# Kernel tuning notes

Hardware: AMD Instinct MI355X
Metric: run time of the kernel (lower is better)

## Reference

```python
import jax, jax.numpy as jnp
import numpy as np

N_NODES = 50000   # num graph nodes
N_EDGES = 800000  # avg degree 16
D = 96            # in_channels == out_channels (residual aggr_out + x)


def setup_inputs() -> dict:
    key = jax.random.key(0)
    k0, k1, k2, k3, k4 = jax.random.split(key, 5)
    x = jax.random.normal(k0, (N_NODES, D), dtype=jnp.float32)
    edge_index = jax.random.randint(k1, (2, N_EDGES), 0, N_NODES)  # [2,E]: row0=src(j), row1=dst(i)
    edge_weight = jax.random.uniform(k2, (N_EDGES,), dtype=jnp.float32)
    pagerank = jax.random.uniform(k3, (N_NODES,), dtype=jnp.float32)
    # nn.Linear(in_channels, out_channels) params
    W = jax.random.normal(k4, (D, D), dtype=jnp.float32) / np.sqrt(D).astype(np.float32)
    b = jnp.zeros((D,), dtype=jnp.float32)
    return {"x": x, "edge_index": edge_index, "edge_weight": edge_weight,
            "pagerank": pagerank, "W": W, "b": b}


def reference(x, edge_index, edge_weight, pagerank, W, b):
    # CGCConv (PyG MessagePassing, aggr='add', flow source_to_target):
    #   message: edge_weight * x_j * pagerank_j   (gather from source nodes)
    #   aggregate: scatter-add to destination nodes
    #   update: Linear(aggr_out + x)
    src = edge_index[0]
    dst = edge_index[1]
    # [E, D] messages: per-edge gather-multiply
    msgs = edge_weight[:, None] * x[src] * pagerank[src][:, None]
    aggr = jax.ops.segment_sum(msgs, dst, num_segments=x.shape[0])  # [N, D]
    return (aggr + x) @ W.T + b
```

## Files before the change

### kernel.cpp

```cpp
#include <hip/hip_runtime.h>


constexpr int NN = 50000;
constexpr int NE = 800000;
constexpr int DD = 96;
constexpr int NB = 196;
constexpr int CAPB = 4608;
constexpr int EPB = 4096;
constexpr int NBLK = (NE + EPB - 1) / EPB;
constexpr int NCVT = (NN * DD / 4 + 511) / 512;

__device__ inline unsigned short f2bf(float f) {
    unsigned u = __float_as_uint(f);
    return (unsigned short)((u + 0x7FFFu + ((u >> 16) & 1u)) >> 16);
}
__device__ inline float bfh(unsigned short v) {
    return __uint_as_float((unsigned)v << 16);
}
__device__ inline unsigned long long pack_e(int meta, float c) {
    return (unsigned long long)(unsigned)meta |
           ((unsigned long long)(unsigned)__float_as_uint(c) << 32);
}

__global__ __launch_bounds__(256) void k_zero(int* __restrict__ cur1) {
    if (threadIdx.x < NB) cur1[threadIdx.x] = 0;
}

__global__ __launch_bounds__(512) void k_prep(const int* __restrict__ src,
                                              const int* __restrict__ dst,
                                              const float* __restrict__ ew,
                                              const float* __restrict__ pr,
                                              int* __restrict__ cur1,
                                              unsigned long long* __restrict__ stage,
                                              const float4* __restrict__ x4,
                                              ushort4* __restrict__ y16v) {
    int tid = threadIdx.x;
    if (blockIdx.x >= NBLK) {
        int i = (blockIdx.x - NBLK) * 512 + tid;
        if (i < NN * DD / 4) {
            float4 v = x4[i];
            y16v[i] = make_ushort4(f2bf(v.x), f2bf(v.y), f2bf(v.z), f2bf(v.w));
        }
        return;
    }
    __shared__ int h[256];
    __shared__ int gb[256];
    __shared__ int sc[256];
    __shared__ unsigned long long sorted[EPB];
    for (int i = tid; i < 256; i += 512) h[i] = 0;
    __syncthreads();
    int base = blockIdx.x * EPB;
    int n = min(EPB, NE - base);

    unsigned long long ent[8]; int bkt[8]; int lrk[8];
    #pragma unroll
    for (int j = 0; j < 8; j++) {
        int e = base + j * 512 + tid;
        bkt[j] = -1;
        if (e < NE) {
            int d = dst[e];
            int s = src[e];
            float c = ew[e] * pr[s];
            int bk = d >> 8;
            bkt[j] = bk;
            lrk[j] = atomicAdd(&h[bk], 1);
            ent[j] = pack_e(s | ((d & 255) << 16) | (bk << 24), c);
        }
    }
    __syncthreads();
    if (tid < 256) sc[tid] = h[tid];
    __syncthreads();
    #pragma unroll
    for (int o = 1; o < 256; o <<= 1) {
        int t = 0;
        if (tid < 256 && tid >= o) t = sc[tid - o];
        __syncthreads();
        if (tid < 256) sc[tid] += t;
        __syncthreads();
    }
    for (int i = tid; i < NB; i += 512)
        gb[i] = h[i] ? atomicAdd(&cur1[i], h[i]) : 0;
    __syncthreads();
    #pragma unroll
    for (int j = 0; j < 8; j++)
        if (bkt[j] >= 0)
            sorted[sc[bkt[j]] - h[bkt[j]] + lrk[j]] = ent[j];
    __syncthreads();
    for (int i = tid; i < n; i += 512) {
        unsigned long long e = sorted[i];
        int bk = ((int)(e >> 24)) & 0xff;
        stage[(size_t)bk * CAPB + gb[bk] + (i - (sc[bk] - h[bk]))] = e;
    }
}

__global__ __launch_bounds__(512) void k_sortB(unsigned long long* __restrict__ stage,
                                               const int* __restrict__ cur1,
                                               int* __restrict__ offs,
                                               int* __restrict__ counts) {
    __shared__ int h[256];
    __shared__ int sc[256];
    __shared__ unsigned sorted[CAPB];
    int b = blockIdx.x;
    int tid = threadIdx.x;
    size_t base = (size_t)b * CAPB;
    int n = cur1[b];

    for (int i = tid; i < 256; i += 512) h[i] = 0;
    __syncthreads();

    unsigned e32[9]; int dl[9]; int lrk[9];
    int m = 0;
    for (int i = tid; i < n; i += 512) {
        unsigned long long e = stage[base + i];
        int dloc = ((int)(e >> 16)) & 0xff;
        unsigned cb = (unsigned)(e >> 32);
        unsigned cbf = (cb + 0x7FFFu + ((cb >> 16) & 1u)) >> 16;
        e32[m] = ((unsigned)e & 0xffffu) | (cbf << 16);
        dl[m] = dloc;
        lrk[m] = atomicAdd(&h[dloc], 1);
        m++;
    }
    __syncthreads();
    if (tid < 256) sc[tid] = h[tid];
    __syncthreads();
    #pragma unroll
    for (int o = 1; o < 256; o <<= 1) {
        int t = 0;
        if (tid < 256 && tid >= o) t = sc[tid - o];
        __syncthreads();
        if (tid < 256) sc[tid] += t;
        __syncthreads();
    }
    m = 0;
    for (int i = tid; i < n; i += 512) {
        sorted[sc[dl[m]] - h[dl[m]] + lrk[m]] = e32[m];
        m++;
    }
    __syncthreads();
    unsigned* outp = (unsigned*)(stage + base);
    for (int i = tid; i < n; i += 512) outp[i] = sorted[i];
    if (tid < 256) {
        int d = (b << 8) + tid;
        if (d < NN) {
            offs[d] = (int)(2 * base) + sc[tid] - h[tid];
            counts[d] = h[tid];
        }
    }
}

__global__ __launch_bounds__(256) void k_pull(const ushort4* __restrict__ y16v,
                                              const float4* __restrict__ x4,
                                              const int* __restrict__ offs,
                                              const int* __restrict__ counts,
                                              const unsigned* __restrict__ ep,
                                              float4* __restrict__ out4) {
    int g = blockIdx.x * 8 + (threadIdx.x >> 5);
    int lane = threadIdx.x & 31;
    if (g >= NN || lane >= 24) return;
    int beg = offs[g];
    int deg = counts[g];
    float ax = 0.f, ay = 0.f, az = 0.f, aw = 0.f;
    int k = 0;
    for (; k + 8 <= deg; k += 8) {
        unsigned e[8];
        #pragma unroll
        for (int j = 0; j < 8; j++) e[j] = ep[beg + k + j];
        ushort4 u[8];
        #pragma unroll
        for (int j = 0; j < 8; j++)
            u[j] = y16v[(size_t)(e[j] & 0xffff) * 24 + lane];
        #pragma unroll
        for (int j = 0; j < 8; j++) {
            float c = bfh((unsigned short)(e[j] >> 16));
            ax += c * bfh(u[j].x);
            ay += c * bfh(u[j].y);
            az += c * bfh(u[j].z);
            aw += c * bfh(u[j].w);
        }
    }
    for (; k + 4 <= deg; k += 4) {
        unsigned e[4];
        #pragma unroll
        for (int j = 0; j < 4; j++) e[j] = ep[beg + k + j];
        ushort4 u[4];
        #pragma unroll
        for (int j = 0; j < 4; j++)
            u[j] = y16v[(size_t)(e[j] & 0xffff) * 24 + lane];
        #pragma unroll
        for (int j = 0; j < 4; j++) {
            float c = bfh((unsigned short)(e[j] >> 16));
            ax += c * bfh(u[j].x);
            ay += c * bfh(u[j].y);
            az += c * bfh(u[j].z);
            aw += c * bfh(u[j].w);
        }
    }
    for (; k < deg; k++) {
        unsigned e = ep[beg + k];
        ushort4 u = y16v[(size_t)(e & 0xffff) * 24 + lane];
        float c = bfh((unsigned short)(e >> 16));
        ax += c * bfh(u.x);
        ay += c * bfh(u.y);
        az += c * bfh(u.z);
        aw += c * bfh(u.w);
    }
    float4 xn = x4[(size_t)g * 24 + lane];
    out4[(size_t)g * 24 + lane] = make_float4(ax + xn.x, ay + xn.y,
                                              az + xn.z, aw + xn.w);
}

constexpr int SWS = 100;
__global__ __launch_bounds__(256, 4) void k_gemm(float* __restrict__ io,
                                                 const float* __restrict__ W,
                                                 const float* __restrict__ b) {
    __shared__ float sWt[DD * SWS];
    int tid = threadIdx.x;
    for (int i = tid; i < DD * DD; i += 256) {
        int o = i / DD, d = i - o * DD;
        sWt[d * SWS + o] = W[i];
    }
    __syncthreads();

    int wave = tid >> 6, lane = tid & 63;
    int og = lane & 7, rgl = lane >> 3;
    int o0 = og * 12;
    int rbase = blockIdx.x * 128 + wave * 32 + rgl;
    const float4* io4 = (const float4*)io;

    int r[4];
    #pragma unroll
    for (int t = 0; t < 4; t++) {
        int rr = rbase + 8 * t;
        r[t] = (rr < NN) ? rr : (NN - 1);
    }

    float acc[4][12];
    #pragma unroll
    for (int t = 0; t < 4; t++)
        #pragma unroll
        for (int m = 0; m < 12; m++) acc[t][m] = 0.f;

    for (int d4 = 0; d4 < 24; d4++) {
        float4 xv[4];
        #pragma unroll
        for (int t = 0; t < 4; t++) xv[t] = io4[(size_t)r[t] * 24 + d4];
        #pragma unroll
        for (int dj = 0; dj < 4; dj++) {
            const float* wp = &sWt[(d4 * 4 + dj) * SWS + o0];
            float4 w0 = *(const float4*)(wp);
            float4 w1 = *(const float4*)(wp + 4);
            float4 w2 = *(const float4*)(wp + 8);
            #pragma unroll
            for (int t = 0; t < 4; t++) {
                float xs = (dj == 0) ? xv[t].x : (dj == 1) ? xv[t].y
                         : (dj == 2) ? xv[t].z : xv[t].w;
                acc[t][0]  += xs * w0.x;  acc[t][1]  += xs * w0.y;
                acc[t][2]  += xs * w0.z;  acc[t][3]  += xs * w0.w;
                acc[t][4]  += xs * w1.x;  acc[t][5]  += xs * w1.y;
                acc[t][6]  += xs * w1.z;  acc[t][7]  += xs * w1.w;
                acc[t][8]  += xs * w2.x;  acc[t][9]  += xs * w2.y;
                acc[t][10] += xs * w2.z;  acc[t][11] += xs * w2.w;
            }
        }
    }

    float4 b0 = *(const float4*)(b + o0);
    float4 b1 = *(const float4*)(b + o0 + 4);
    float4 b2 = *(const float4*)(b + o0 + 8);
    float4* io4w = (float4*)io;
    #pragma unroll
    for (int t = 0; t < 4; t++) {
        int rr = rbase + 8 * t;
        if (rr < NN) {
            size_t base = (size_t)rr * 24 + og * 3;
            io4w[base + 0] = make_float4(acc[t][0] + b0.x, acc[t][1] + b0.y,
                                         acc[t][2] + b0.z, acc[t][3] + b0.w);
            io4w[base + 1] = make_float4(acc[t][4] + b1.x, acc[t][5] + b1.y,
                                         acc[t][6] + b1.z, acc[t][7] + b1.w);
            io4w[base + 2] = make_float4(acc[t][8] + b2.x, acc[t][9] + b2.y,
                                         acc[t][10] + b2.z, acc[t][11] + b2.w);
        }
    }
}

extern "C" void kernel_launch(void* const* d_in, const int* in_sizes, int n_in,
                              void* d_out, int out_size, void* d_ws, size_t ws_size,
                              hipStream_t stream) {
    const float* x  = (const float*)d_in[0];
    const int*   ei = (const int*)d_in[1];
    const float* ew = (const float*)d_in[2];
    const float* pr = (const float*)d_in[3];
    const float* W  = (const float*)d_in[4];
    const float* b  = (const float*)d_in[5];
    float* out = (float*)d_out;

    unsigned long long* stage = (unsigned long long*)d_ws;
    unsigned short* y16 = (unsigned short*)(stage + (size_t)NB * CAPB);
    int* cur1   = (int*)(y16 + (size_t)NN * DD);
    int* offs   = cur1 + NB;
    int* counts = offs + NN;

    const int* src = ei;
    const int* dst = ei + NE;

    k_zero<<<1, 256, 0, stream>>>(cur1);
    k_prep<<<NBLK + NCVT, 512, 0, stream>>>(src, dst, ew, pr, cur1, stage,
                                            (const float4*)x, (ushort4*)y16);
    k_sortB<<<NB, 512, 0, stream>>>(stage, cur1, offs, counts);
    k_pull<<<(NN + 7) / 8, 256, 0, stream>>>((const ushort4*)y16, (const float4*)x,
                                             offs, counts, (const unsigned*)stage,
                                             (float4*)out);
    k_gemm<<<(NN + 127) / 128, 256, 0, stream>>>(out, W, b);
}
```

Baseline: 151.0 us.

## Use bf16 MFMA for the dense linear and store the aggregation in bf16

The pull kernel now writes aggr+x as bf16 into a workspace buffer instead of fp32 into the output. The GEMM kernel is rewritten to use 16x16x32 bf16 MFMA instructions, with W converted to bf16 and laid out in MFMA B-fragment order in shared memory, and it writes fp32 results straight to the output. This halves the intermediate traffic and moves the 96x96 matmul off scalar FMA onto matrix cores, at the cost of bf16 rounding of both the activations and the weights.

```diff
diff --git a/kernel.cpp b/kernel.cpp
--- a/kernel.cpp
+++ b/kernel.cpp
@@ -9,6 +9,9 @@
 constexpr int EPB = 4096;
 constexpr int NBLK = (NE + EPB - 1) / EPB;
 constexpr int NCVT = (NN * DD / 4 + 511) / 512;
+
+using s8v = __attribute__((ext_vector_type(8))) short;
+using f4v = __attribute__((ext_vector_type(4))) float;
 
 __device__ inline unsigned short f2bf(float f) {
     unsigned u = __float_as_uint(f);
@@ -153,7 +156,7 @@
                                               const int* __restrict__ offs,
                                               const int* __restrict__ counts,
                                               const unsigned* __restrict__ ep,
-                                              float4* __restrict__ out4) {
+                                              ushort4* __restrict__ io16v) {
     int g = blockIdx.x * 8 + (threadIdx.x >> 5);
     int lane = threadIdx.x & 31;
     if (g >= NN || lane >= 24) return;
@@ -205,80 +208,54 @@
         aw += c * bfh(u.w);
     }
     float4 xn = x4[(size_t)g * 24 + lane];
-    out4[(size_t)g * 24 + lane] = make_float4(ax + xn.x, ay + xn.y,
-                                              az + xn.z, aw + xn.w);
-}
-
-constexpr int SWS = 100;
-__global__ __launch_bounds__(256, 4) void k_gemm(float* __restrict__ io,
-                                                 const float* __restrict__ W,
-                                                 const float* __restrict__ b) {
-    __shared__ float sWt[DD * SWS];
+    io16v[(size_t)g * 24 + lane] = make_ushort4(f2bf(ax + xn.x), f2bf(ay + xn.y),
+                                                f2bf(az + xn.z), f2bf(aw + xn.w));
+}
+
+__global__ __launch_bounds__(256) void k_gemm(const unsigned short* __restrict__ io16,
+                                              const float* __restrict__ W,
+                                              const float* __restrict__ b,
+                                              float* __restrict__ out) {
+    __shared__ short bfr[18 * 64 * 8];
     int tid = threadIdx.x;
-    for (int i = tid; i < DD * DD; i += 256) {
-        int o = i / DD, d = i - o * DD;
-        sWt[d * SWS + o] = W[i];
+    for (int i = tid; i < 18 * 512; i += 256) {
+        int f = i >> 9, r = i & 511;
+        int lane = r >> 3, j = r & 7;
+        int ks = f / 6, nt = f - 6 * ks;
+        int n = nt * 16 + (lane & 15);
+        int k = ks * 32 + (lane >> 4) * 8 + j;
+        bfr[i] = (short)f2bf(W[n * DD + k]);
     }
     __syncthreads();
 
     int wave = tid >> 6, lane = tid & 63;
-    int og = lane & 7, rgl = lane >> 3;
-    int o0 = og * 12;
-    int rbase = blockIdx.x * 128 + wave * 32 + rgl;
-    const float4* io4 = (const float4*)io;
-
-    int r[4];
-    #pragma unroll
-    for (int t = 0; t < 4; t++) {
-        int rr = rbase + 8 * t;
-        r[t] = (rr < NN) ? rr : (NN - 1);
-    }
-
-    float acc[4][12];
-    #pragma unroll
-    for (int t = 0; t < 4; t++)
-        #pragma unroll
-        for (int m = 0; m < 12; m++) acc[t][m] = 0.f;
-
-    for (int d4 = 0; d4 < 24; d4++) {
-        float4 xv[4];
-        #pragma unroll
-        for (int t = 0; t < 4; t++) xv[t] = io4[(size_t)r[t] * 24 + d4];
-        #pragma unroll
-        for (int dj = 0; dj < 4; dj++) {
-            const float* wp = &sWt[(d4 * 4 + dj) * SWS + o0];
-            float4 w0 = *(const float4*)(wp);
-            float4 w1 = *(const float4*)(wp + 4);
-            float4 w2 = *(const float4*)(wp + 8);
-            #pragma unroll
-            for (int t = 0; t < 4; t++) {
-                float xs = (dj == 0) ? xv[t].x : (dj == 1) ? xv[t].y
-                         : (dj == 2) ? xv[t].z : xv[t].w;
-                acc[t][0]  += xs * w0.x;  acc[t][1]  += xs * w0.y;
-                acc[t][2]  += xs * w0.z;  acc[t][3]  += xs * w0.w;
-                acc[t][4]  += xs * w1.x;  acc[t][5]  += xs * w1.y;
-                acc[t][6]  += xs * w1.z;  acc[t][7]  += xs * w1.w;
-                acc[t][8]  += xs * w2.x;  acc[t][9]  += xs * w2.y;
-                acc[t][10] += xs * w2.z;  acc[t][11] += xs * w2.w;
-            }
-        }
-    }
-
-    float4 b0 = *(const float4*)(b + o0);
-    float4 b1 = *(const float4*)(b + o0 + 4);
-    float4 b2 = *(const float4*)(b + o0 + 8);
-    float4* io4w = (float4*)io;
-    #pragma unroll
-    for (int t = 0; t < 4; t++) {
-        int rr = rbase + 8 * t;
-        if (rr < NN) {
-            size_t base = (size_t)rr * 24 + og * 3;
-            io4w[base + 0] = make_float4(acc[t][0] + b0.x, acc[t][1] + b0.y,
-                                         acc[t][2] + b0.z, acc[t][3] + b0.w);
-            io4w[base + 1] = make_float4(acc[t][4] + b1.x, acc[t][5] + b1.y,
-                                         acc[t][6] + b1.z, acc[t][7] + b1.w);
-            io4w[base + 2] = make_float4(acc[t][8] + b2.x, acc[t][9] + b2.y,
-                                         acc[t][10] + b2.z, acc[t][11] + b2.w);
+    int quad = lane >> 4, m16 = lane & 15;
+    int r0 = blockIdx.x * 64 + wave * 16;
+    int rowa = r0 + m16;
+    if (rowa >= NN) rowa = NN - 1;
+
+    f4v acc[6];
+    #pragma unroll
+    for (int nt = 0; nt < 6; nt++) acc[nt] = (f4v){0.f, 0.f, 0.f, 0.f};
+
+    #pragma unroll
+    for (int ks = 0; ks < 3; ks++) {
+        s8v a = *(const s8v*)(io16 + (size_t)rowa * DD + ks * 32 + quad * 8);
+        #pragma unroll
+        for (int nt = 0; nt < 6; nt++) {
+            s8v bb = *(const s8v*)&bfr[((ks * 6 + nt) * 64 + lane) * 8];
+            acc[nt] = __builtin_amdgcn_mfma_f32_16x16x32_bf16(a, bb, acc[nt], 0, 0, 0);
+        }
+    }
+
+    #pragma unroll
+    for (int nt = 0; nt < 6; nt++) {
+        float bias = b[nt * 16 + m16];
+        #pragma unroll
+        for (int reg = 0; reg < 4; reg++) {
+            int rr = r0 + quad * 4 + reg;
+            if (rr < NN)
+                out[(size_t)rr * DD + nt * 16 + m16] = acc[nt][reg] + bias;
         }
     }
 }
@@ -299,6 +276,7 @@
     int* cur1   = (int*)(y16 + (size_t)NN * DD);
     int* offs   = cur1 + NB;
     int* counts = offs + NN;
+    unsigned short* io16 = (unsigned short*)(counts + NN);
 
     const int* src = ei;
     const int* dst = ei + NE;
@@ -309,6 +287,6 @@
     k_sortB<<<NB, 512, 0, stream>>>(stage, cur1, offs, counts);
     k_pull<<<(NN + 7) / 8, 256, 0, stream>>>((const ushort4*)y16, (const float4*)x,
                                              offs, counts, (const unsigned*)stage,
-                                             (float4*)out);
-    k_gemm<<<(NN + 127) / 128, 256, 0, stream>>>(out, W, b);
-}
+                                             (ushort4*)io16);
+    k_gemm<<<(NN + 63) / 64, 256, 0, stream>>>(io16, W, b, out);
+}
```

Result: faster. 141.5 us (-6.3%).
